# Kernel optimization log

Hardware: AMD Instinct MI355X
Metric: run time of the kernel (lower is better)

## Reference

```python
import jax, jax.numpy as jnp
import numpy as np

B, C, H, W, E, R, TOP_K = 8, 128, 128, 128, 4, 64, 2


def setup_inputs() -> dict:
    key = jax.random.key(0)
    ks = jax.random.split(key, 12)
    s = 0.02
    return {
        "x": jax.random.normal(ks[0], (B, C, H, W), jnp.float32),
        "shared": jax.random.normal(ks[1], (B, C, H, W), jnp.float32),
        # FrequencyEmbedding MLP: Linear(C,2C) -> GELU -> Linear(2C,C)
        "mlp_w1": jax.random.normal(ks[2], (C, 2 * C), jnp.float32) * s,
        "mlp_b1": jnp.zeros((2 * C,), jnp.float32),
        "mlp_w2": jax.random.normal(ks[3], (2 * C, C), jnp.float32) * s,
        "mlp_b2": jnp.zeros((C,), jnp.float32),
        # routing gates: Linear(C,E) on pooled x, Linear(C,E) on freq emb
        "gate_w": jax.random.normal(ks[4], (C, E), jnp.float32) * s,
        "freq_gate_w": jax.random.normal(ks[5], (C, E), jnp.float32) * s,
        # per-expert 1x1 conv weights (ModExpert.proj, expert_layer=Identity)
        "exp_w0": jax.random.normal(ks[6], (E, R, C), jnp.float32) * s,  # dim->rank
        "exp_w1": jax.random.normal(ks[7], (E, R, C), jnp.float32) * s,  # dim->rank (on shared)
        "exp_w2": jax.random.normal(ks[8], (E, C, R), jnp.float32) * s,  # rank->dim
        # AdapterLayer.proj_out 1x1 conv
        "proj_w": jax.random.normal(ks[9], (C, C), jnp.float32) * s,
    }


def reference(x, shared, mlp_w1, mlp_b1, mlp_w2, mlp_b2, gate_w, freq_gate_w,
              exp_w0, exp_w1, exp_w2, proj_w):
    b, c = x.shape[0], x.shape[1]
    # --- FrequencyEmbedding: frozen depthwise high-pass 3x3 -> GELU -> mean(HW) -> MLP ---
    hp = jnp.array([[-1., -1., -1.], [-1., 8., -1.], [-1., -1., -1.]], dtype=x.dtype)
    kern = jnp.broadcast_to(hp, (c, 1, 3, 3))
    h = jax.lax.conv_general_dilated(
        x, kern, window_strides=(1, 1), padding='SAME',
        feature_group_count=c, dimension_numbers=('NCHW', 'OIHW', 'NCHW'))
    h = jax.nn.gelu(h, approximate=False)
    fe = h.mean(axis=(-2, -1))                                    # [B, C]
    fe = jax.nn.gelu(fe @ mlp_w1 + mlp_b1, approximate=False) @ mlp_w2 + mlp_b2
    # --- RoutingFunction (eval / noiseless): softmax -> top-k -> scatter gates ---
    pooled = x.mean(axis=(-2, -1))                                # [B, C]
    logits = pooled @ gate_w + fe @ freq_gate_w                   # [B, E]
    scores = jax.nn.softmax(logits, axis=-1)
    vals, idx = jax.lax.top_k(scores, TOP_K)
    gates = jnp.zeros_like(scores).at[jnp.arange(b)[:, None], idx].set(vals)  # [B, E]
    # --- Experts (dense equivalent of SparseDispatcher gather->expert->scatter-add) ---
    # expert_e(x, shared) = x + W2_e @ ((W0_e @ x) * silu(W1_e @ shared))
    a = jnp.einsum('bchw,erc->berhw', x, exp_w0)                  # [B,E,R,H,W]
    g = jax.nn.silu(jnp.einsum('bchw,erc->berhw', shared, exp_w1))
    y = jnp.einsum('berhw,edr->bedhw', a * g, exp_w2)             # [B,E,C,H,W]
    # gated combine; residual shortcut enters once per selected expert, weighted by gate
    out = jnp.einsum('be,bedhw->bdhw', gates, y) + gates.sum(axis=1)[:, None, None, None] * x
    # --- proj_out 1x1 ---
    return jnp.einsum('bchw,dc->bdhw', out, proj_w)
```

## Files before the change

### kernel.cpp

```cpp
#include <hip/hip_runtime.h>
#include <hip/hip_bf16.h>
#include <math.h>

#define CC   128
#define HWN  16384
#define EE   4
#define RR   64
#define TP   64
#define NT   (HWN / TP)

typedef __attribute__((ext_vector_type(8))) short short8;
typedef __attribute__((ext_vector_type(4))) float f32x4;

__device__ __forceinline__ unsigned short f2bf(float f) {
    __hip_bfloat16 h = __float2bfloat16(f);
    return *reinterpret_cast<unsigned short*>(&h);
}
__device__ __forceinline__ unsigned pk2bf(float lo, float hi) {
    return (unsigned)f2bf(lo) | ((unsigned)f2bf(hi) << 16);
}
__device__ __forceinline__ float gelu_exact(float v) {
    return 0.5f * v * (1.0f + erff(v * 0.7071067811865475f));
}
__device__ __forceinline__ float silu_f(float v) {
    return v / (1.0f + expf(-v));
}

#define PREP_CONV 1024
#define PREP_WCV  (PREP_CONV + 128)
#define PREP_WF   (PREP_WCV + 128)
#define PREP_TR   (PREP_WF + 1024)
#define PREP_GRID (PREP_TR + 48)
__global__ __launch_bounds__(256) void k_prep(
    const float* __restrict__ x,   const float* __restrict__ sh,
    const float* __restrict__ proj,
    const float* __restrict__ ew0, const float* __restrict__ ew1,
    const float* __restrict__ ew2,
    const float* __restrict__ mw1, const float* __restrict__ mw2,
    const float* __restrict__ gw,  const float* __restrict__ fgw,
    float* __restrict__ fe0, float* __restrict__ pooled,
    unsigned short* __restrict__ projb, unsigned short* __restrict__ w0b,
    unsigned short* __restrict__ w1b,   unsigned short* __restrict__ w2pb,
    float* __restrict__ outw, float* __restrict__ dummy)
{
    __shared__ float wred[8];
    const int bx = blockIdx.x, tid = threadIdx.x;

    if (bx < PREP_CONV) {
        const int bc = bx;
        const float* base = x + (size_t)bc * HWN;
        const int r  = tid >> 1;
        const int c0 = (tid & 1) << 6;
        const float* rm = base + r * 128 + c0;
        const float* rt = rm - 128;
        const float* rb = rm + 128;
        const bool hT = (r > 0), hB = (r < 127);
        float tl, ml, bl;
        if (c0 == 0) { tl = ml = bl = 0.f; }
        else         { tl = hT ? rt[-1] : 0.f; ml = rm[-1]; bl = hB ? rb[-1] : 0.f; }
        float4 tC = hT ? ((const float4*)rt)[0] : (float4){0.f,0.f,0.f,0.f};
        float4 mC = ((const float4*)rm)[0];
        float4 bC = hB ? ((const float4*)rb)[0] : (float4){0.f,0.f,0.f,0.f};
        float sg = 0.f, sx = 0.f;
        #pragma unroll
        for (int j = 0; j < 16; ++j) {
            float4 tN, mN, bN;
            if (j < 15) {
                tN = hT ? ((const float4*)rt)[j + 1] : (float4){0.f,0.f,0.f,0.f};
                mN = ((const float4*)rm)[j + 1];
                bN = hB ? ((const float4*)rb)[j + 1] : (float4){0.f,0.f,0.f,0.f};
            } else {
                float tr_ = 0.f, mr_ = 0.f, br_ = 0.f;
                if (c0 == 0) { tr_ = hT ? rt[64] : 0.f; mr_ = rm[64]; br_ = hB ? rb[64] : 0.f; }
                tN = (float4){tr_,0.f,0.f,0.f}; mN = (float4){mr_,0.f,0.f,0.f}; bN = (float4){br_,0.f,0.f,0.f};
            }
            const float tA[6] = {tl, tC.x, tC.y, tC.z, tC.w, tN.x};
            const float mA[6] = {ml, mC.x, mC.y, mC.z, mC.w, mN.x};
            const float bA[6] = {bl, bC.x, bC.y, bC.z, bC.w, bN.x};
            #pragma unroll
            for (int k = 0; k < 4; ++k) {
                float s8 = ((tA[k] + tA[k+1]) + (tA[k+2] + mA[k]))
                         + ((mA[k+2] + bA[k]) + (bA[k+1] + bA[k+2]));
                sg += gelu_exact(8.f * mA[k+1] - s8);
                sx += mA[k+1];
            }
            tl = tC.w; ml = mC.w; bl = bC.w; tC = tN; mC = mN; bC = bN;
        }
        for (int off = 32; off > 0; off >>= 1) {
            sg += __shfl_down(sg, off, 64);
            sx += __shfl_down(sx, off, 64);
        }
        if ((tid & 63) == 0) { wred[tid >> 6] = sg; wred[4 + (tid >> 6)] = sx; }
        __syncthreads();
        if (tid == 0) {
            fe0[bc]    = (wred[0] + wred[1] + wred[2] + wred[3]) * (1.f / 16384.f);
            pooled[bc] = (wred[4] + wred[5] + wred[6] + wred[7]) * (1.f / 16384.f);
        }
    } else if (bx < PREP_WCV) {
        int i = (bx - PREP_CONV) * 256 + tid;
        if (i < CC * CC) projb[i] = f2bf(proj[i]);
        w0b[i] = f2bf(ew0[i]);
        w1b[i] = f2bf(ew1[i]);
    } else if (bx < PREP_WF) {
        const int bb = bx - PREP_WCV;
        const int e  = bb >> 5;
        const int d  = ((bb & 31) << 2) + (tid >> 6);
        const int r  = tid & 63;
        const float* pr = proj + d * CC;
        const float* wz = ew2 + (size_t)e * CC * RR + r;
        float a0 = 0.f, a1 = 0.f, a2 = 0.f, a3 = 0.f;
        for (int c = 0; c < CC; c += 4) {
            a0 += pr[c + 0] * wz[(c + 0) * RR];
            a1 += pr[c + 1] * wz[(c + 1) * RR];
            a2 += pr[c + 2] * wz[(c + 2) * RR];
            a3 += pr[c + 3] * wz[(c + 3) * RR];
        }
        w2pb[(e * CC + d) * RR + r] = f2bf((a0 + a1) + (a2 + a3));
    } else if (bx < PREP_TR) {
        const int idx = bx - PREP_WF;
        const int d   = idx & 127;
        const int b   = idx >> 7;
        const float* s0 = (d < 64)
            ? x  + ((size_t)b * CC + 2 * d) * HWN
            : sh + ((size_t)b * CC + 2 * (d - 64)) * HWN;
        const float4* a4 = (const float4*)s0;
        const float4* c4 = (const float4*)(s0 + HWN);
        uint4* dst = (uint4*)((unsigned*)outw + ((size_t)b * CC + d) * HWN);
        for (int i = tid; i < HWN / 4; i += 256) {
            float4 a = a4[i], c = c4[i];
            uint4 w;
            w.x = pk2bf(a.x, c.x);
            w.y = pk2bf(a.y, c.y);
            w.z = pk2bf(a.z, c.z);
            w.w = pk2bf(a.w, c.w);
            dst[i] = w;
        }
    } else {
        const int i = (bx - PREP_TR) * 256 + tid;
        float s = 0.f;
        for (int j = i; j < CC * 2 * CC; j += 48 * 256) s += mw1[j] + mw2[j];
        if (i < CC * EE) s += gw[i] + fgw[i];
        if (s == 12345.678f) dummy[1] = s;
    }
}

__global__ __launch_bounds__(256) void k_route(
    const float* __restrict__ fe0, const float* __restrict__ pooled,
    const float* __restrict__ w1, const float* __restrict__ b1,
    const float* __restrict__ w2, const float* __restrict__ b2,
    const float* __restrict__ gw, const float* __restrict__ fgw,
    float* __restrict__ gates, float* __restrict__ gsum)
{
    const int b = blockIdx.x, tid = threadIdx.x;
    __shared__ float hh[256];
    __shared__ float fe[128];
    __shared__ float lg[4];
    {
        const float* f0 = fe0 + b * CC;
        float a[8];
        #pragma unroll
        for (int j = 0; j < 8; ++j) a[j] = 0.f;
        for (int c = 0; c < CC; c += 8)
            #pragma unroll
            for (int j = 0; j < 8; ++j) a[j] += f0[c + j] * w1[(c + j) * 256 + tid];
        float acc = b1[tid] + ((a[0]+a[1]) + (a[2]+a[3])) + ((a[4]+a[5]) + (a[6]+a[7]));
        hh[tid] = gelu_exact(acc);
    }
    __syncthreads();
    if (tid < 128) {
        float a[8];
        #pragma unroll
        for (int j = 0; j < 8; ++j) a[j] = 0.f;
        for (int c = 0; c < 256; c += 8)
            #pragma unroll
            for (int j = 0; j < 8; ++j) a[j] += hh[c + j] * w2[(c + j) * 128 + tid];
        fe[tid] = b2[tid] + ((a[0]+a[1]) + (a[2]+a[3])) + ((a[4]+a[5]) + (a[6]+a[7]));
    }
    __syncthreads();
    if (tid < EE) {
        const float* pl = pooled + b * CC;
        float l0=0.f, l1=0.f, l2=0.f, l3=0.f;
        for (int c = 0; c < CC; c += 4) {
            l0 += pl[c+0] * gw[(c+0) * EE + tid] + fe[c+0] * fgw[(c+0) * EE + tid];
            l1 += pl[c+1] * gw[(c+1) * EE + tid] + fe[c+1] * fgw[(c+1) * EE + tid];
            l2 += pl[c+2] * gw[(c+2) * EE + tid] + fe[c+2] * fgw[(c+2) * EE + tid];
            l3 += pl[c+3] * gw[(c+3) * EE + tid] + fe[c+3] * fgw[(c+3) * EE + tid];
        }
        lg[tid] = (l0 + l1) + (l2 + l3);
    }
    __syncthreads();
    if (tid == 0) {
        float mx = fmaxf(fmaxf(lg[0], lg[1]), fmaxf(lg[2], lg[3]));
        float sc[EE]; float ssum = 0.f;
        for (int e = 0; e < EE; ++e) { sc[e] = expf(lg[e] - mx); ssum += sc[e]; }
        float inv = 1.f / ssum;
        for (int e = 0; e < EE; ++e) sc[e] *= inv;
        int i1 = 0;
        for (int e = 1; e < EE; ++e) if (sc[e] > sc[i1]) i1 = e;
        int i2 = -1;
        for (int e = 0; e < EE; ++e) {
            if (e == i1) continue;
            if (i2 < 0 || sc[e] > sc[i2]) i2 = e;
        }
        for (int e = 0; e < EE; ++e)
            gates[b * EE + e] = (e == i1) ? sc[i1] : (e == i2 ? sc[i2] : 0.f);
        gsum[b] = sc[i1] + sc[i2];
    }
}

__global__ __launch_bounds__(256, 4) void k_experts(
    const unsigned short* __restrict__ w0b, const unsigned short* __restrict__ w1b,
    const unsigned short* __restrict__ w2pb, const unsigned short* __restrict__ projb,
    const float* __restrict__ gates, const float* __restrict__ gsum,
    float* __restrict__ out)
{
    __shared__ __align__(16) unsigned short xs [TP * CC];
    __shared__ __align__(16) unsigned short shs[TP * CC];
    __shared__ __align__(16) unsigned short us [TP * RR];
    const int tid  = threadIdx.x;
    const int b    = blockIdx.x >> 8;
    const int tile = blockIdx.x & (NT - 1);
    const int p0   = tile * TP;

    {
        const unsigned* wsrc = (const unsigned*)out + ((size_t)b * CC) * HWN + p0;
        const int p  = tid & 63;
        const int qh = tid >> 6;
        #pragma unroll
        for (int it = 0; it < 4; ++it) {
            const int q  = it * 4 + qh;
            const int sw = p * CC + ((q ^ (p & 15)) << 3);
            const unsigned* px_ = wsrc + (size_t)(q * 4) * HWN + p;
            const unsigned* ps_ = wsrc + (size_t)(64 + q * 4) * HWN + p;
            uint4 wx, wh;
            wx.x = px_[0]; wx.y = px_[HWN]; wx.z = px_[2 * HWN]; wx.w = px_[3 * HWN];
            wh.x = ps_[0]; wh.y = ps_[HWN]; wh.z = ps_[2 * HWN]; wh.w = ps_[3 * HWN];
            *(uint4*)&xs [sw] = wx;
            *(uint4*)&shs[sw] = wh;
        }
    }
    __syncthreads();

    const int wv = tid >> 6;
    const int ln = tid & 63;
    const int lp = ln & 15;
    const int lq = ln >> 4;

    f32x4 acc[2][4];
    #pragma unroll
    for (int i = 0; i < 2; ++i)
        #pragma unroll
        for (int j = 0; j < 4; ++j) acc[i][j] = (f32x4){0.f, 0.f, 0.f, 0.f};

    {
        const int d0 = wv * 32;
        #pragma unroll
        for (int ks = 0; ks < 4; ++ks) {
            const int k0 = ks * 32 + lq * 8;
            const int ch = ks * 4 + lq;
            short8 a0 = *(const short8*)&projb[(d0 +      lp) * CC + k0];
            short8 a1 = *(const short8*)&projb[(d0 + 16 + lp) * CC + k0];
            #pragma unroll
            for (int pt = 0; pt < 4; ++pt) {
                short8 bf = *(const short8*)&xs[(pt * 16 + lp) * CC + ((ch ^ lp) << 3)];
                acc[0][pt] = __builtin_amdgcn_mfma_f32_16x16x32_bf16(a0, bf, acc[0][pt], 0, 0, 0);
                acc[1][pt] = __builtin_amdgcn_mfma_f32_16x16x32_bf16(a1, bf, acc[1][pt], 0, 0, 0);
            }
        }
        const float gs = gsum[b];
        #pragma unroll
        for (int i = 0; i < 2; ++i)
            #pragma unroll
            for (int j = 0; j < 4; ++j) acc[i][j] *= gs;
    }

    for (int e = 0; e < EE; ++e) {
        const float ge = gates[b * EE + e];
        if (ge == 0.f) continue;

        f32x4 af[4], gf[4];
        #pragma unroll
        for (int pt = 0; pt < 4; ++pt) { af[pt] = (f32x4){0.f,0.f,0.f,0.f}; gf[pt] = (f32x4){0.f,0.f,0.f,0.f}; }
        const unsigned short* w0e = w0b + (size_t)(e * RR + wv * 16) * CC;
        const unsigned short* w1e = w1b + (size_t)(e * RR + wv * 16) * CC;
        #pragma unroll
        for (int ks = 0; ks < 4; ++ks) {
            const int k0 = ks * 32 + lq * 8;
            const int ch = ks * 4 + lq;
            short8 a0 = *(const short8*)&w0e[lp * CC + k0];
            short8 a1 = *(const short8*)&w1e[lp * CC + k0];
            #pragma unroll
            for (int pt = 0; pt < 4; ++pt) {
                const int sw = (pt * 16 + lp) * CC + ((ch ^ lp) << 3);
                short8 bx = *(const short8*)&xs [sw];
                short8 bs = *(const short8*)&shs[sw];
                af[pt] = __builtin_amdgcn_mfma_f32_16x16x32_bf16(a0, bx, af[pt], 0, 0, 0);
                gf[pt] = __builtin_amdgcn_mfma_f32_16x16x32_bf16(a1, bs, gf[pt], 0, 0, 0);
            }
        }
        __syncthreads();
        #pragma unroll
        for (int pt = 0; pt < 4; ++pt) {
            unsigned short t[4];
            #pragma unroll
            for (int i = 0; i < 4; ++i)
                t[i] = f2bf(ge * af[pt][i] * silu_f(gf[pt][i]));
            const int p = pt * 16 + lp;
            const int addr = p * RR + (((wv * 2 + (lq >> 1)) ^ (lp & 7)) << 3) + ((lq & 1) << 2);
            *(uint2*)&us[addr] = *(uint2*)t;
        }
        __syncthreads();
        const unsigned short* w2e = w2pb + (size_t)(e * CC + wv * 32) * RR;
        #pragma unroll
        for (int ks = 0; ks < 2; ++ks) {
            const int k0 = ks * 32 + lq * 8;
            const int ch = ks * 4 + lq;
            short8 a0 = *(const short8*)&w2e[lp * RR + k0];
            short8 a1 = *(const short8*)&w2e[(16 + lp) * RR + k0];
            #pragma unroll
            for (int pt = 0; pt < 4; ++pt) {
                short8 bu = *(const short8*)&us[(pt * 16 + lp) * RR + ((ch ^ (lp & 7)) << 3)];
                acc[0][pt] = __builtin_amdgcn_mfma_f32_16x16x32_bf16(a0, bu, acc[0][pt], 0, 0, 0);
                acc[1][pt] = __builtin_amdgcn_mfma_f32_16x16x32_bf16(a1, bu, acc[1][pt], 0, 0, 0);
            }
        }
    }

    {
        const int d0 = wv * 32;
        #pragma unroll
        for (int dt = 0; dt < 2; ++dt)
            #pragma unroll
            for (int pt = 0; pt < 4; ++pt) {
                float* ob = out + ((size_t)(b * CC + d0 + dt * 16 + lq * 4)) * HWN + p0 + pt * 16 + lp;
                #pragma unroll
                for (int i = 0; i < 4; ++i)
                    ob[(size_t)i * HWN] = acc[dt][pt][i];
            }
    }
}

extern "C" void kernel_launch(void* const* d_in, const int* in_sizes, int n_in,
                              void* d_out, int out_size, void* d_ws, size_t ws_size,
                              hipStream_t stream) {
    const float* x    = (const float*)d_in[0];
    const float* shr  = (const float*)d_in[1];
    const float* mw1  = (const float*)d_in[2];
    const float* mb1  = (const float*)d_in[3];
    const float* mw2  = (const float*)d_in[4];
    const float* mb2  = (const float*)d_in[5];
    const float* gw   = (const float*)d_in[6];
    const float* fgw  = (const float*)d_in[7];
    const float* ew0  = (const float*)d_in[8];
    const float* ew1  = (const float*)d_in[9];
    const float* ew2  = (const float*)d_in[10];
    const float* pw   = (const float*)d_in[11];
    float* out = (float*)d_out;

    float* ws     = (float*)d_ws;
    float* fe0    = ws + 0;
    float* pooled = ws + 1024;
    float* gates  = ws + 2048;
    float* gsum   = ws + 2080;
    float* dummy  = ws + 2088;
    unsigned short* projb = (unsigned short*)(ws + 2112);
    unsigned short* w0b   = projb + 16384;
    unsigned short* w1b   = w0b + 32768;
    unsigned short* w2pb  = w1b + 32768;

    k_prep   <<<PREP_GRID, 256, 0, stream>>>(x, shr, pw, ew0, ew1, ew2, mw1, mw2,
                                             gw, fgw, fe0, pooled, projb, w0b, w1b, w2pb,
                                             out, dummy);
    k_route  <<<8,         256, 0, stream>>>(fe0, pooled, mw1, mb1, mw2, mb2, gw, fgw, gates, gsum);
    k_experts<<<8 * NT,    256, 0, stream>>>(w0b, w1b, w2pb, projb, gates, gsum, out);
}
```

Baseline: 296.1 us.

## Fuse x bf16 packing into the high-pass conv pass to read x once

The depthwise high-pass conv and mean reduction now also write the packed bf16 channel-pair layout of x, so x is read from global memory once instead of twice. Each block handles a channel pair for one batch, with warps walking 32 rows each as a rolling three-row stencil and neighbours exchanged via shuffles. Separate blocks still pack the shared input. The cost is more shuffles per row and fewer, heavier conv blocks (512 instead of 1024), which lowers parallelism.

Measured after the change: 259.4 us. 1.14x faster.

```diff
diff --git a/kernel.cpp b/kernel.cpp
--- a/kernel.cpp
+++ b/kernel.cpp
@@ -26,11 +26,11 @@
     return v / (1.0f + expf(-v));
 }
 
-#define PREP_CONV 1024
-#define PREP_WCV  (PREP_CONV + 128)
+#define PREP_CVX  512
+#define PREP_SHP  (PREP_CVX + 512)
+#define PREP_WCV  (PREP_SHP + 128)
 #define PREP_WF   (PREP_WCV + 128)
-#define PREP_TR   (PREP_WF + 1024)
-#define PREP_GRID (PREP_TR + 48)
+#define PREP_GRID (PREP_WF + 48)
 __global__ __launch_bounds__(256) void k_prep(
     const float* __restrict__ x,   const float* __restrict__ sh,
     const float* __restrict__ proj,
@@ -43,61 +43,94 @@
     unsigned short* __restrict__ w1b,   unsigned short* __restrict__ w2pb,
     float* __restrict__ outw, float* __restrict__ dummy)
 {
-    __shared__ float wred[8];
+    __shared__ float wr2[2][2][4];
     const int bx = blockIdx.x, tid = threadIdx.x;
 
-    if (bx < PREP_CONV) {
-        const int bc = bx;
-        const float* base = x + (size_t)bc * HWN;
-        const int r  = tid >> 1;
-        const int c0 = (tid & 1) << 6;
-        const float* rm = base + r * 128 + c0;
-        const float* rt = rm - 128;
-        const float* rb = rm + 128;
-        const bool hT = (r > 0), hB = (r < 127);
-        float tl, ml, bl;
-        if (c0 == 0) { tl = ml = bl = 0.f; }
-        else         { tl = hT ? rt[-1] : 0.f; ml = rm[-1]; bl = hB ? rb[-1] : 0.f; }
-        float4 tC = hT ? ((const float4*)rt)[0] : (float4){0.f,0.f,0.f,0.f};
-        float4 mC = ((const float4*)rm)[0];
-        float4 bC = hB ? ((const float4*)rb)[0] : (float4){0.f,0.f,0.f,0.f};
+    if (bx < PREP_CVX) {
+        const int dpr  = bx & 63;
+        const int b    = bx >> 6;
+        const int ln   = tid & 63;
+        const int wv   = tid >> 6;
+        const int half = ln >> 5;
+        const int c4   = (ln & 31) << 2;
+        const float* src = x + ((size_t)(b * CC + 2 * dpr + half)) * HWN + c4;
+        unsigned* dst = (unsigned*)outw + ((size_t)(b * CC + dpr)) * HWN + c4;
+        const int r0 = wv << 5;
+
+        const float4 z4 = {0.f, 0.f, 0.f, 0.f};
+        float4 t4 = z4, m4, b4;
+        float tl = 0.f, tr = 0.f, ml, mr, bl, br;
+        if (r0 > 0) {
+            t4 = *(const float4*)(src + (size_t)(r0 - 1) * 128);
+            tl = __shfl(t4.w, ln - 1, 64); if ((ln & 31) == 0)  tl = 0.f;
+            tr = __shfl(t4.x, ln + 1, 64); if ((ln & 31) == 31) tr = 0.f;
+        }
+        m4 = *(const float4*)(src + (size_t)r0 * 128);
+        ml = __shfl(m4.w, ln - 1, 64); if ((ln & 31) == 0)  ml = 0.f;
+        mr = __shfl(m4.x, ln + 1, 64); if ((ln & 31) == 31) mr = 0.f;
+
         float sg = 0.f, sx = 0.f;
-        #pragma unroll
-        for (int j = 0; j < 16; ++j) {
-            float4 tN, mN, bN;
-            if (j < 15) {
-                tN = hT ? ((const float4*)rt)[j + 1] : (float4){0.f,0.f,0.f,0.f};
-                mN = ((const float4*)rm)[j + 1];
-                bN = hB ? ((const float4*)rb)[j + 1] : (float4){0.f,0.f,0.f,0.f};
-            } else {
-                float tr_ = 0.f, mr_ = 0.f, br_ = 0.f;
-                if (c0 == 0) { tr_ = hT ? rt[64] : 0.f; mr_ = rm[64]; br_ = hB ? rb[64] : 0.f; }
-                tN = (float4){tr_,0.f,0.f,0.f}; mN = (float4){mr_,0.f,0.f,0.f}; bN = (float4){br_,0.f,0.f,0.f};
-            }
-            const float tA[6] = {tl, tC.x, tC.y, tC.z, tC.w, tN.x};
-            const float mA[6] = {ml, mC.x, mC.y, mC.z, mC.w, mN.x};
-            const float bA[6] = {bl, bC.x, bC.y, bC.z, bC.w, bN.x};
+        for (int g = r0; g < r0 + 32; ++g) {
+            if (g + 1 < 128) {
+                b4 = *(const float4*)(src + (size_t)(g + 1) * 128);
+                bl = __shfl(b4.w, ln - 1, 64); if ((ln & 31) == 0)  bl = 0.f;
+                br = __shfl(b4.x, ln + 1, 64); if ((ln & 31) == 31) br = 0.f;
+            } else { b4 = z4; bl = 0.f; br = 0.f; }
+            const float ta[6] = {tl, t4.x, t4.y, t4.z, t4.w, tr};
+            const float ma[6] = {ml, m4.x, m4.y, m4.z, m4.w, mr};
+            const float ba[6] = {bl, b4.x, b4.y, b4.z, b4.w, br};
             #pragma unroll
             for (int k = 0; k < 4; ++k) {
-                float s8 = ((tA[k] + tA[k+1]) + (tA[k+2] + mA[k]))
-                         + ((mA[k+2] + bA[k]) + (bA[k+1] + bA[k+2]));
-                sg += gelu_exact(8.f * mA[k+1] - s8);
-                sx += mA[k+1];
-            }
-            tl = tC.w; ml = mC.w; bl = bC.w; tC = tN; mC = mN; bC = bN;
-        }
-        for (int off = 32; off > 0; off >>= 1) {
-            sg += __shfl_down(sg, off, 64);
-            sx += __shfl_down(sx, off, 64);
-        }
-        if ((tid & 63) == 0) { wred[tid >> 6] = sg; wred[4 + (tid >> 6)] = sx; }
+                float s8 = ((ta[k] + ta[k+1]) + (ta[k+2] + ma[k]))
+                         + ((ma[k+2] + ba[k]) + (ba[k+1] + ba[k+2]));
+                sg += gelu_exact(8.f * ma[k+1] - s8);
+                sx += ma[k+1];
+            }
+            float ox = __shfl(m4.x, ln ^ 32, 64);
+            float oy = __shfl(m4.y, ln ^ 32, 64);
+            float oz = __shfl(m4.z, ln ^ 32, 64);
+            float ow = __shfl(m4.w, ln ^ 32, 64);
+            if (half == 0) {
+                uint4 w;
+                w.x = pk2bf(m4.x, ox); w.y = pk2bf(m4.y, oy);
+                w.z = pk2bf(m4.z, oz); w.w = pk2bf(m4.w, ow);
+                *(uint4*)(dst + (size_t)g * 128) = w;
+            }
+            t4 = m4; tl = ml; tr = mr;
+            m4 = b4; ml = bl; mr = br;
+        }
+        #pragma unroll
+        for (int off = 16; off; off >>= 1) {
+            sg += __shfl_xor(sg, off, 64);
+            sx += __shfl_xor(sx, off, 64);
+        }
+        if ((ln & 31) == 0) { wr2[half][0][wv] = sg; wr2[half][1][wv] = sx; }
         __syncthreads();
-        if (tid == 0) {
-            fe0[bc]    = (wred[0] + wred[1] + wred[2] + wred[3]) * (1.f / 16384.f);
-            pooled[bc] = (wred[4] + wred[5] + wred[6] + wred[7]) * (1.f / 16384.f);
+        if (tid < 2) {
+            float g4 = (wr2[tid][0][0] + wr2[tid][0][1]) + (wr2[tid][0][2] + wr2[tid][0][3]);
+            float x4 = (wr2[tid][1][0] + wr2[tid][1][1]) + (wr2[tid][1][2] + wr2[tid][1][3]);
+            fe0   [b * CC + 2 * dpr + tid] = g4 * (1.f / 16384.f);
+            pooled[b * CC + 2 * dpr + tid] = x4 * (1.f / 16384.f);
+        }
+    } else if (bx < PREP_SHP) {
+        const int idx = bx - PREP_CVX;
+        const int dpr = idx & 63;
+        const int b   = idx >> 6;
+        const float* s0 = sh + ((size_t)b * CC + 2 * dpr) * HWN;
+        const float4* a4 = (const float4*)s0;
+        const float4* c4p = (const float4*)(s0 + HWN);
+        uint4* dst = (uint4*)((unsigned*)outw + ((size_t)(b * CC + 64 + dpr)) * HWN);
+        for (int i = tid; i < HWN / 4; i += 256) {
+            float4 a = a4[i], c = c4p[i];
+            uint4 w;
+            w.x = pk2bf(a.x, c.x);
+            w.y = pk2bf(a.y, c.y);
+            w.z = pk2bf(a.z, c.z);
+            w.w = pk2bf(a.w, c.w);
+            dst[i] = w;
         }
     } else if (bx < PREP_WCV) {
-        int i = (bx - PREP_CONV) * 256 + tid;
+        int i = (bx - PREP_SHP) * 256 + tid;
         if (i < CC * CC) projb[i] = f2bf(proj[i]);
         w0b[i] = f2bf(ew0[i]);
         w1b[i] = f2bf(ew1[i]);
@@ -116,27 +149,8 @@
             a3 += pr[c + 3] * wz[(c + 3) * RR];
         }
         w2pb[(e * CC + d) * RR + r] = f2bf((a0 + a1) + (a2 + a3));
-    } else if (bx < PREP_TR) {
-        const int idx = bx - PREP_WF;
-        const int d   = idx & 127;
-        const int b   = idx >> 7;
-        const float* s0 = (d < 64)
-            ? x  + ((size_t)b * CC + 2 * d) * HWN
-            : sh + ((size_t)b * CC + 2 * (d - 64)) * HWN;
-        const float4* a4 = (const float4*)s0;
-        const float4* c4 = (const float4*)(s0 + HWN);
-        uint4* dst = (uint4*)((unsigned*)outw + ((size_t)b * CC + d) * HWN);
-        for (int i = tid; i < HWN / 4; i += 256) {
-            float4 a = a4[i], c = c4[i];
-            uint4 w;
-            w.x = pk2bf(a.x, c.x);
-            w.y = pk2bf(a.y, c.y);
-            w.z = pk2bf(a.z, c.z);
-            w.w = pk2bf(a.w, c.w);
-            dst[i] = w;
-        }
     } else {
-        const int i = (bx - PREP_TR) * 256 + tid;
+        const int i = (bx - PREP_WF) * 256 + tid;
         float s = 0.f;
         for (int j = i; j < CC * 2 * CC; j += 48 * 256) s += mw1[j] + mw2[j];
         if (i < CC * EE) s += gw[i] + fgw[i];
```
